# Kernel optimization log

Measured on AMD Instinct MI355X. Metric: run time of the kernel, lower is better.

## Reference

```python
import jax, jax.numpy as jnp
import numpy as np

N_FREQS = 6  # PositionEmbedding N_freqs when embedding=='pe'

def _pe(x):
    freqs = (2.0 ** jnp.arange(N_FREQS)).astype(x.dtype)
    fx = x * freqs  # [B,Q,N_FREQS]
    sc = jnp.stack([jnp.sin(fx), jnp.cos(fx)], axis=-1).reshape(fx.shape[0], fx.shape[1], 2 * N_FREQS)
    return jnp.concatenate([x, sc], axis=-1)

def _mlp(h, W1, b1, W2, b2, W3, b3):
    h = jax.nn.relu(h @ W1 + b1)
    h = jax.nn.relu(h @ W2 + b2)
    return h @ W3 + b3

def setup_inputs() -> dict:
    key = jax.random.key(0)
    B, Q, N, D, H = 4, 65536, 8192, 16, 128
    ks = jax.random.split(key, 6)
    coord = jax.random.uniform(ks[0], (B, Q, 1), minval=-1.0, maxval=1.0, dtype=jnp.float32)
    latent = jax.random.normal(ks[1], (B, N, D), dtype=jnp.float32)
    in_dim = (1 + 2 * N_FREQS) + 3 * D  # pe(rel_coord) ++ unfolded feat = 13 + 48 = 61
    def init(k, shp, fan):
        return (jax.random.normal(k, shp, dtype=jnp.float32) / np.float32(np.sqrt(fan)))
    W1 = init(ks[2], (in_dim, H), in_dim); b1 = jnp.zeros((H,), jnp.float32)
    W2 = init(ks[3], (H, H), H);          b2 = jnp.zeros((H,), jnp.float32)
    W3 = init(ks[4], (H, 1), H);          b3 = jnp.zeros((1,), jnp.float32)
    return dict(coord=coord, latent=latent, W1=W1, b1=b1, W2=W2, b2=b2, W3=W3, b3=b3)

def reference(coord, latent, W1, b1, W2, b2, W3, b3):
    B, Q, _ = coord.shape
    N = latent.shape[1]
    # feat_unfold: concat shifted-prev / self / shifted-next along feature dim -> [B,N,3D]
    prev = jnp.concatenate([latent[:, :1], latent[:, :-1]], axis=1)
    nxt = jnp.concatenate([latent[:, 1:], latent[:, -1:]], axis=1)
    feat = jnp.concatenate([prev, latent, nxt], axis=-1)
    # make_coord grid: cell centers in [-1,1]
    grid = (-1.0 + (2.0 * jnp.arange(N, dtype=coord.dtype) + 1.0) / N)
    rx = 1.0 / N           # 2/num_latents/2
    eps_shift = 1e-6
    preds, areas = [], []
    for vx in (-2.0, 0.0):  # eval path vx_lst
        c = jnp.clip(coord + vx * rx + eps_shift, -1.0 + 1e-6, 1.0 - 1e-6)
        idx = jnp.clip(jnp.searchsorted(grid, c[..., 0]), 0, N - 1)  # [B,Q]
        q_coord = grid[idx][..., None]                               # [B,Q,1]
        q_feat = jnp.take_along_axis(feat, idx[..., None], axis=1)   # [B,Q,3D]
        rel = (coord - q_coord) * N                                  # scaled rel coord
        area = jnp.abs(rel[..., 0]) + 1e-9                           # [B,Q]
        inp = jnp.concatenate([_pe(rel), q_feat], axis=-1)           # [B,Q,61]
        preds.append(_mlp(inp, W1, b1, W2, b2, W3, b3))              # [B,Q,1]
        areas.append(area)
    tot = areas[0] + areas[1]
    # local_ensemble: swap areas before weighting
    ret = preds[0] * (areas[1] / tot)[..., None] + preds[1] * (areas[0] / tot)[..., None]
    return ret
```

## Files before the change

kernel.cpp:

```cpp
#include <hip/hip_runtime.h>
#include <hip/hip_bf16.h>

typedef short s8v __attribute__((ext_vector_type(8)));
typedef float f4v __attribute__((ext_vector_type(4)));
typedef unsigned u4v __attribute__((ext_vector_type(4)));

__device__ __forceinline__ unsigned short f2bf(float x) {
  unsigned u = __builtin_bit_cast(unsigned, x);
  u += 0x7fffu + ((u >> 16) & 1u);
  return (unsigned short)(u >> 16);
}
__device__ __forceinline__ unsigned pk2(float a, float b) {
  unsigned ua = __builtin_bit_cast(unsigned, a) + 0x8000u;
  unsigned ub = __builtin_bit_cast(unsigned, b) + 0x8000u;
  return __builtin_amdgcn_perm(ub, ua, 0x07060302u);
}

__global__ void prep_kernel(const float* __restrict__ W1, const float* __restrict__ b1,
                            const float* __restrict__ W2, unsigned short* __restrict__ wsW) {
  int e = blockIdx.x * 256 + threadIdx.x;
  if (e < 8192) {
    int frag = e >> 9, rem = e & 511, lane = rem >> 3, j = rem & 7;
    int h = frag >> 1, ks = frag & 1;
    int q4 = lane >> 4, l15 = lane & 15;
    int k = ks * 32 + q4 * 8 + j;
    int n = h * 16 + l15;
    float v;
    if (k < 13) v = W1[k * 128 + n];
    else if (k == 13) v = b1[n];
    else if (k < 16) v = 0.0f;
    else v = W1[(k - 3) * 128 + n];
    wsW[e] = f2bf(v);
  } else {
    int e2 = e - 8192;
    int frag = e2 >> 9, rem = e2 & 511, lane = rem >> 3, j = rem & 7;
    int h2 = frag >> 2, ks = frag & 3;
    int q4 = lane >> 4, l15 = lane & 15;
    int kd = (j < 4) ? (32 * ks + 4 * q4 + j) : (32 * ks + 16 + 4 * q4 + (j - 4));
    int n = h2 * 16 + l15;
    wsW[e] = f2bf(W2[kd * 128 + n]);
  }
}

__global__ __launch_bounds__(256, 2) void lisagon_main(
    const float* __restrict__ coord, const float* __restrict__ latent,
    const unsigned short* __restrict__ W1f, const unsigned short* __restrict__ W2f,
    const float* __restrict__ b2, const float* __restrict__ W3,
    const float* __restrict__ b3, float* __restrict__ out) {
  __shared__ __align__(16) unsigned short A1[256 * 64];
  __shared__ float AREA[256];

  const int t = threadIdx.x;
  const int lane = t & 63, wv = t >> 6;
  const int l15 = lane & 15, q4 = lane >> 4;

  {
    const int r = t;
    const int Rg = blockIdx.x * 256 + r;
    const int gq = Rg >> 1, p = Rg & 1;
    const float co = coord[gq];
    float c = (co + (p ? 0.0f : -0.000244140625f)) + 1e-6f;
    c = fminf(fmaxf(c, -1.0f + 1e-6f), 1.0f - 1e-6f);
    double u = ((double)c * 8192.0 + 8191.0) * 0.5;
    int idx = (int)ceil(u);
    idx = min(max(idx, 0), 8191);

    float qc = ((float)(2 * idx + 1) - 8192.0f) * (1.0f / 8192.0f);
    float rel = (co - qc) * 8192.0f;
    AREA[r] = fabsf(rel) + 1e-9f;

    uint4* A1v = (uint4*)A1;
    const float4* latv = (const float4*)(latent + (size_t)(gq >> 16) * (8192 * 16));
    int rows3[3];
    rows3[0] = max(idx - 1, 0);
    rows3[1] = idx;
    rows3[2] = min(idx + 1, 8191);
    float4 L[3][4];
#pragma unroll
    for (int s = 0; s < 3; s++)
#pragma unroll
      for (int w = 0; w < 4; w++) L[s][w] = latv[rows3[s] * 4 + w];

    float v[16];
    v[0] = rel;
    float f = rel;
#pragma unroll
    for (int i = 0; i < 6; i++) {
      v[1 + 2 * i] = __sinf(f);
      v[2 + 2 * i] = __cosf(f);
      f = f + f;
    }
    v[13] = 1.0f;
    v[14] = 0.0f; v[15] = 0.0f;
#pragma unroll
    for (int ch = 0; ch < 2; ch++) {
      union { uint4 u4; unsigned us[4]; } pkv;
#pragma unroll
      for (int w = 0; w < 4; w++) pkv.us[w] = pk2(v[ch * 8 + 2 * w], v[ch * 8 + 2 * w + 1]);
      A1v[r * 8 + (ch ^ (r & 7))] = pkv.u4;
    }
#pragma unroll
    for (int s = 0; s < 3; s++) {
      union { uint4 u4; unsigned us[4]; } p0, p1;
      p0.us[0] = pk2(L[s][0].x, L[s][0].y); p0.us[1] = pk2(L[s][0].z, L[s][0].w);
      p0.us[2] = pk2(L[s][1].x, L[s][1].y); p0.us[3] = pk2(L[s][1].z, L[s][1].w);
      p1.us[0] = pk2(L[s][2].x, L[s][2].y); p1.us[1] = pk2(L[s][2].z, L[s][2].w);
      p1.us[2] = pk2(L[s][3].x, L[s][3].y); p1.us[3] = pk2(L[s][3].z, L[s][3].w);
      int ch0 = 2 + 2 * s;
      A1v[r * 8 + (ch0 ^ (r & 7))]       = p0.u4;
      A1v[r * 8 + ((ch0 + 1) ^ (r & 7))] = p1.u4;
    }
  }
  __syncthreads();

  const s8v* W1fv = (const s8v*)W1f;
  const s8v* W2fv = (const s8v*)W2f;
  const s8v* A1s  = (const s8v*)A1;
  const int rbase = wv * 64;

  s8v Bf[2][4];
#pragma unroll
  for (int ks = 0; ks < 2; ks++)
#pragma unroll
    for (int rt = 0; rt < 4; rt++) {
      int row = rbase + rt * 16 + l15;
      Bf[ks][rt] = A1s[row * 8 + ((ks * 4 + q4) ^ (row & 7))];
    }

  u4v bbv[4][4];
#pragma unroll
  for (int h = 0; h < 8; h++) {
    f4v a[4];
#pragma unroll
    for (int rt = 0; rt < 4; rt++) a[rt] = (f4v){0.f, 0.f, 0.f, 0.f};
#pragma unroll
    for (int ks = 0; ks < 2; ks++) {
      s8v Af = W1fv[(h * 2 + ks) * 64 + lane];
#pragma unroll
      for (int rt = 0; rt < 4; rt++)
        a[rt] = __builtin_amdgcn_mfma_f32_16x16x32_bf16(Af, Bf[ks][rt], a[rt], 0, 0, 0);
    }
#pragma unroll
    for (int rt = 0; rt < 4; rt++) {
      bbv[rt][h >> 1][2 * (h & 1)]     = pk2(fmaxf(a[rt][0], 0.f), fmaxf(a[rt][1], 0.f));
      bbv[rt][h >> 1][2 * (h & 1) + 1] = pk2(fmaxf(a[rt][2], 0.f), fmaxf(a[rt][3], 0.f));
    }
  }

  float s[4] = {0.f, 0.f, 0.f, 0.f};
#pragma unroll
  for (int h2 = 0; h2 < 8; h2++) {
    f4v a2[4];
    f4v b2v = ((const f4v*)b2)[h2 * 4 + q4];
#pragma unroll
    for (int rt = 0; rt < 4; rt++) a2[rt] = b2v;
#pragma unroll
    for (int ks = 0; ks < 4; ks++) {
      s8v Af = W2fv[(h2 * 4 + ks) * 64 + lane];
#pragma unroll
      for (int rt = 0; rt < 4; rt++)
        a2[rt] = __builtin_amdgcn_mfma_f32_16x16x32_bf16(
            Af, __builtin_bit_cast(s8v, bbv[rt][ks]), a2[rt], 0, 0, 0);
    }
    float4 w3v = ((const float4*)W3)[h2 * 4 + q4];
#pragma unroll
    for (int rt = 0; rt < 4; rt++) {
      s[rt] += fmaxf(a2[rt][0], 0.f) * w3v.x;
      s[rt] += fmaxf(a2[rt][1], 0.f) * w3v.y;
      s[rt] += fmaxf(a2[rt][2], 0.f) * w3v.z;
      s[rt] += fmaxf(a2[rt][3], 0.f) * w3v.w;
    }
  }

  const float b3s = b3[0];
#pragma unroll
  for (int rt = 0; rt < 4; rt++) {
    float pred = s[rt];
    pred += __shfl_xor(pred, 16, 64);
    pred += __shfl_xor(pred, 32, 64);
    pred += b3s;
    float other = __shfl_xor(pred, 1, 64);
    if (q4 == 0 && (l15 & 1) == 0) {
      int row0 = rbase + rt * 16 + l15;
      float a0 = AREA[row0], a1 = AREA[row0 + 1];
      float tot = a0 + a1;
      out[(blockIdx.x * 256 + row0) >> 1] = pred * (a1 / tot) + other * (a0 / tot);
    }
  }
}

extern "C" void kernel_launch(void* const* d_in, const int* in_sizes, int n_in,
                              void* d_out, int out_size, void* d_ws, size_t ws_size,
                              hipStream_t stream) {
  const float* coord  = (const float*)d_in[0];
  const float* latent = (const float*)d_in[1];
  const float* W1 = (const float*)d_in[2];
  const float* b1 = (const float*)d_in[3];
  const float* W2 = (const float*)d_in[4];
  const float* b2 = (const float*)d_in[5];
  const float* W3 = (const float*)d_in[6];
  const float* b3 = (const float*)d_in[7];
  float* out = (float*)d_out;
  unsigned short* wsW = (unsigned short*)d_ws;

  prep_kernel<<<96, 256, 0, stream>>>(W1, b1, W2, wsW);
  lisagon_main<<<2048, 256, 0, stream>>>(coord, latent, wsW, wsW + 8192,
                                         b2, W3, b3, out);
}
```

Baseline: 104.9 us.

## Switch MLP matmuls from 16x16x32 to 32x32x16 bf16 MFMA tiles

Replaces the 16x16x32 MFMA tiling of both hidden layers with 32x32x16 MFMA instructions. The weight-prep kernel and the register layouts for the layer-1 output, the bias, W3 and the final reduction are re-derived to match. Larger MFMA tiles mean fewer instructions and fewer weight-fragment loads per row, at the cost of more accumulator registers per wave and a less flexible layout that may affect occupancy.

```diff
diff --git a/kernel.cpp b/kernel.cpp
--- a/kernel.cpp
+++ b/kernel.cpp
@@ -2,7 +2,7 @@
 #include <hip/hip_bf16.h>
 
 typedef short s8v __attribute__((ext_vector_type(8)));
-typedef float f4v __attribute__((ext_vector_type(4)));
+typedef float f16v __attribute__((ext_vector_type(16)));
 typedef unsigned u4v __attribute__((ext_vector_type(4)));
 
 __device__ __forceinline__ unsigned short f2bf(float x) {
@@ -21,10 +21,10 @@
   int e = blockIdx.x * 256 + threadIdx.x;
   if (e < 8192) {
     int frag = e >> 9, rem = e & 511, lane = rem >> 3, j = rem & 7;
-    int h = frag >> 1, ks = frag & 1;
-    int q4 = lane >> 4, l15 = lane & 15;
-    int k = ks * 32 + q4 * 8 + j;
-    int n = h * 16 + l15;
+    int mt = frag >> 2, ks = frag & 3;
+    int half = lane >> 5, m = lane & 31;
+    int k = 16 * ks + 8 * half + j;
+    int n = 32 * mt + m;
     float v;
     if (k < 13) v = W1[k * 128 + n];
     else if (k == 13) v = b1[n];
@@ -34,11 +34,11 @@
   } else {
     int e2 = e - 8192;
     int frag = e2 >> 9, rem = e2 & 511, lane = rem >> 3, j = rem & 7;
-    int h2 = frag >> 2, ks = frag & 3;
-    int q4 = lane >> 4, l15 = lane & 15;
-    int kd = (j < 4) ? (32 * ks + 4 * q4 + j) : (32 * ks + 16 + 4 * q4 + (j - 4));
-    int n = h2 * 16 + l15;
-    wsW[e] = f2bf(W2[kd * 128 + n]);
+    int mt2 = frag >> 3, ks = frag & 7;
+    int half = lane >> 5, m = lane & 31;
+    int h = 32 * (ks >> 1) + 4 * half + (j & 3) + 8 * (j >> 2) + ((ks & 1) ? 16 : 0);
+    int n = 32 * mt2 + m;
+    wsW[e] = f2bf(W2[h * 128 + n]);
   }
 }
 
@@ -52,7 +52,7 @@
 
   const int t = threadIdx.x;
   const int lane = t & 63, wv = t >> 6;
-  const int l15 = lane & 15, q4 = lane >> 4;
+  const int l31 = lane & 31, half = lane >> 5;
 
   {
     const int r = t;
@@ -118,73 +118,86 @@
   const s8v* A1s  = (const s8v*)A1;
   const int rbase = wv * 64;
 
-  s8v Bf[2][4];
-#pragma unroll
-  for (int ks = 0; ks < 2; ks++)
-#pragma unroll
-    for (int rt = 0; rt < 4; rt++) {
-      int row = rbase + rt * 16 + l15;
-      Bf[ks][rt] = A1s[row * 8 + ((ks * 4 + q4) ^ (row & 7))];
-    }
-
-  u4v bbv[4][4];
-#pragma unroll
-  for (int h = 0; h < 8; h++) {
-    f4v a[4];
-#pragma unroll
-    for (int rt = 0; rt < 4; rt++) a[rt] = (f4v){0.f, 0.f, 0.f, 0.f};
-#pragma unroll
-    for (int ks = 0; ks < 2; ks++) {
-      s8v Af = W1fv[(h * 2 + ks) * 64 + lane];
-#pragma unroll
-      for (int rt = 0; rt < 4; rt++)
-        a[rt] = __builtin_amdgcn_mfma_f32_16x16x32_bf16(Af, Bf[ks][rt], a[rt], 0, 0, 0);
-    }
-#pragma unroll
-    for (int rt = 0; rt < 4; rt++) {
-      bbv[rt][h >> 1][2 * (h & 1)]     = pk2(fmaxf(a[rt][0], 0.f), fmaxf(a[rt][1], 0.f));
-      bbv[rt][h >> 1][2 * (h & 1) + 1] = pk2(fmaxf(a[rt][2], 0.f), fmaxf(a[rt][3], 0.f));
-    }
-  }
-
-  float s[4] = {0.f, 0.f, 0.f, 0.f};
-#pragma unroll
-  for (int h2 = 0; h2 < 8; h2++) {
-    f4v a2[4];
-    f4v b2v = ((const f4v*)b2)[h2 * 4 + q4];
-#pragma unroll
-    for (int rt = 0; rt < 4; rt++) a2[rt] = b2v;
+  s8v Bin[2][4];
+#pragma unroll
+  for (int nt = 0; nt < 2; nt++)
 #pragma unroll
     for (int ks = 0; ks < 4; ks++) {
-      s8v Af = W2fv[(h2 * 4 + ks) * 64 + lane];
-#pragma unroll
-      for (int rt = 0; rt < 4; rt++)
-        a2[rt] = __builtin_amdgcn_mfma_f32_16x16x32_bf16(
-            Af, __builtin_bit_cast(s8v, bbv[rt][ks]), a2[rt], 0, 0, 0);
-    }
-    float4 w3v = ((const float4*)W3)[h2 * 4 + q4];
-#pragma unroll
-    for (int rt = 0; rt < 4; rt++) {
-      s[rt] += fmaxf(a2[rt][0], 0.f) * w3v.x;
-      s[rt] += fmaxf(a2[rt][1], 0.f) * w3v.y;
-      s[rt] += fmaxf(a2[rt][2], 0.f) * w3v.z;
-      s[rt] += fmaxf(a2[rt][3], 0.f) * w3v.w;
+      int row = rbase + nt * 32 + l31;
+      int o = 2 * ks + half;
+      Bin[nt][ks] = A1s[row * 8 + (o ^ (row & 7))];
+    }
+
+  u4v bbv[2][8];
+#pragma unroll
+  for (int mt = 0; mt < 4; mt++) {
+    f16v a[2];
+#pragma unroll
+    for (int nt = 0; nt < 2; nt++) a[nt] = (f16v)0.0f;
+#pragma unroll
+    for (int ks = 0; ks < 4; ks++) {
+      s8v Af = W1fv[(mt * 4 + ks) * 64 + lane];
+#pragma unroll
+      for (int nt = 0; nt < 2; nt++)
+        a[nt] = __builtin_amdgcn_mfma_f32_32x32x16_bf16(Af, Bin[nt][ks], a[nt], 0, 0, 0);
+    }
+#pragma unroll
+    for (int nt = 0; nt < 2; nt++) {
+#pragma unroll
+      for (int w = 0; w < 4; w++) {
+        bbv[nt][2 * mt][w] =
+            pk2(fmaxf(a[nt][2 * w], 0.f), fmaxf(a[nt][2 * w + 1], 0.f));
+        bbv[nt][2 * mt + 1][w] =
+            pk2(fmaxf(a[nt][8 + 2 * w], 0.f), fmaxf(a[nt][9 + 2 * w], 0.f));
+      }
+    }
+  }
+
+  float s[2] = {0.f, 0.f};
+#pragma unroll
+  for (int mt2 = 0; mt2 < 4; mt2++) {
+    f16v a2i;
+#pragma unroll
+    for (int g = 0; g < 4; g++) {
+      float4 b2g = *(const float4*)(b2 + 32 * mt2 + 4 * half + 8 * g);
+      a2i[4 * g + 0] = b2g.x; a2i[4 * g + 1] = b2g.y;
+      a2i[4 * g + 2] = b2g.z; a2i[4 * g + 3] = b2g.w;
+    }
+    f16v a2[2];
+    a2[0] = a2i; a2[1] = a2i;
+#pragma unroll
+    for (int ks = 0; ks < 8; ks++) {
+      s8v Af = W2fv[(mt2 * 8 + ks) * 64 + lane];
+#pragma unroll
+      for (int nt = 0; nt < 2; nt++)
+        a2[nt] = __builtin_amdgcn_mfma_f32_32x32x16_bf16(
+            Af, __builtin_bit_cast(s8v, bbv[nt][ks]), a2[nt], 0, 0, 0);
+    }
+#pragma unroll
+    for (int g = 0; g < 4; g++) {
+      float4 w3g = *(const float4*)(W3 + 32 * mt2 + 4 * half + 8 * g);
+#pragma unroll
+      for (int nt = 0; nt < 2; nt++) {
+        s[nt] += fmaxf(a2[nt][4 * g + 0], 0.f) * w3g.x;
+        s[nt] += fmaxf(a2[nt][4 * g + 1], 0.f) * w3g.y;
+        s[nt] += fmaxf(a2[nt][4 * g + 2], 0.f) * w3g.z;
+        s[nt] += fmaxf(a2[nt][4 * g + 3], 0.f) * w3g.w;
+      }
     }
   }
 
   const float b3s = b3[0];
 #pragma unroll
-  for (int rt = 0; rt < 4; rt++) {
-    float pred = s[rt];
-    pred += __shfl_xor(pred, 16, 64);
+  for (int nt = 0; nt < 2; nt++) {
+    float pred = s[nt];
     pred += __shfl_xor(pred, 32, 64);
     pred += b3s;
     float other = __shfl_xor(pred, 1, 64);
-    if (q4 == 0 && (l15 & 1) == 0) {
-      int row0 = rbase + rt * 16 + l15;
-      float a0 = AREA[row0], a1 = AREA[row0 + 1];
+    if (half == 0 && (l31 & 1) == 0) {
+      int rloc = rbase + nt * 32 + l31;
+      float a0 = AREA[rloc], a1 = AREA[rloc + 1];
       float tot = a0 + a1;
-      out[(blockIdx.x * 256 + row0) >> 1] = pred * (a1 / tot) + other * (a0 / tot);
+      out[(blockIdx.x * 256 + rloc) >> 1] = pred * (a1 / tot) + other * (a0 / tot);
     }
   }
 }
```

Result: slower. 120.8 us (+15.1%).

## Pre-convert latent to bf16, stage W2 in LDS, use hardware bf16 pack

Applied to the files above, without the earlier changes.

The prep kernel now also converts the whole latent tensor to bf16 in the workspace, so the main kernel gathers half as many bytes per neighbour row and no longer packs them itself. W2 fragments are copied into shared memory with global_load_lds at kernel start, and the second-layer MFMA loop reads them from LDS instead of global memory. pk2 uses the hardware cvt_pk_bf16_f32 builtin when the compiler provides it. The cost is a larger prep launch that reads and writes all of latent, plus an extra 32 KB of LDS per block, which may limit blocks per CU. There is no explicit wait on the async LDS copy beyond the existing __syncthreads.

```diff
diff --git a/kernel.cpp b/kernel.cpp
--- a/kernel.cpp
+++ b/kernel.cpp
@@ -10,14 +10,27 @@
   u += 0x7fffu + ((u >> 16) & 1u);
   return (unsigned short)(u >> 16);
 }
+#if __has_builtin(__builtin_amdgcn_cvt_pk_bf16_f32)
+__device__ __forceinline__ unsigned pk2(float a, float b) {
+  return __builtin_bit_cast(unsigned, __builtin_amdgcn_cvt_pk_bf16_f32(a, b));
+}
+#else
 __device__ __forceinline__ unsigned pk2(float a, float b) {
   unsigned ua = __builtin_bit_cast(unsigned, a) + 0x8000u;
   unsigned ub = __builtin_bit_cast(unsigned, b) + 0x8000u;
   return __builtin_amdgcn_perm(ub, ua, 0x07060302u);
 }
+#endif
+
+__device__ __forceinline__ void g2lds16(const void* g, void* l) {
+  __builtin_amdgcn_global_load_lds(
+      (const __attribute__((address_space(1))) unsigned*)g,
+      (__attribute__((address_space(3))) unsigned*)l, 16, 0, 0);
+}
 
 __global__ void prep_kernel(const float* __restrict__ W1, const float* __restrict__ b1,
-                            const float* __restrict__ W2, unsigned short* __restrict__ wsW) {
+                            const float* __restrict__ W2, const float* __restrict__ latent,
+                            unsigned short* __restrict__ wsW) {
   int e = blockIdx.x * 256 + threadIdx.x;
   if (e < 8192) {
     int frag = e >> 9, rem = e & 511, lane = rem >> 3, j = rem & 7;
@@ -31,7 +44,7 @@
     else if (k < 16) v = 0.0f;
     else v = W1[(k - 3) * 128 + n];
     wsW[e] = f2bf(v);
-  } else {
+  } else if (e < 24576) {
     int e2 = e - 8192;
     int frag = e2 >> 9, rem = e2 & 511, lane = rem >> 3, j = rem & 7;
     int h2 = frag >> 2, ks = frag & 3;
@@ -39,20 +52,30 @@
     int kd = (j < 4) ? (32 * ks + 4 * q4 + j) : (32 * ks + 16 + 4 * q4 + (j - 4));
     int n = h2 * 16 + l15;
     wsW[e] = f2bf(W2[kd * 128 + n]);
+  } else {
+    int i = e - 24576;
+    wsW[e] = f2bf(latent[i]);
   }
 }
 
 __global__ __launch_bounds__(256, 2) void lisagon_main(
-    const float* __restrict__ coord, const float* __restrict__ latent,
+    const float* __restrict__ coord, const unsigned short* __restrict__ latbf,
     const unsigned short* __restrict__ W1f, const unsigned short* __restrict__ W2f,
     const float* __restrict__ b2, const float* __restrict__ W3,
     const float* __restrict__ b3, float* __restrict__ out) {
   __shared__ __align__(16) unsigned short A1[256 * 64];
+  __shared__ __align__(16) unsigned short W2s[16384];
   __shared__ float AREA[256];
 
   const int t = threadIdx.x;
   const int lane = t & 63, wv = t >> 6;
   const int l15 = lane & 15, q4 = lane >> 4;
+
+#pragma unroll
+  for (int it = 0; it < 8; it++) {
+    int off = (it * 4 + wv) * 1024;
+    g2lds16((const char*)W2f + off + lane * 16, (char*)W2s + off);
+  }
 
   {
     const int r = t;
@@ -70,16 +93,17 @@
     AREA[r] = fabsf(rel) + 1e-9f;
 
     uint4* A1v = (uint4*)A1;
-    const float4* latv = (const float4*)(latent + (size_t)(gq >> 16) * (8192 * 16));
+    const uint4* latv = (const uint4*)(latbf + (size_t)(gq >> 16) * (8192 * 16));
     int rows3[3];
     rows3[0] = max(idx - 1, 0);
     rows3[1] = idx;
     rows3[2] = min(idx + 1, 8191);
-    float4 L[3][4];
-#pragma unroll
-    for (int s = 0; s < 3; s++)
-#pragma unroll
-      for (int w = 0; w < 4; w++) L[s][w] = latv[rows3[s] * 4 + w];
+    uint4 L0[3], L1[3];
+#pragma unroll
+    for (int s = 0; s < 3; s++) {
+      L0[s] = latv[rows3[s] * 2 + 0];
+      L1[s] = latv[rows3[s] * 2 + 1];
+    }
 
     float v[16];
     v[0] = rel;
@@ -101,20 +125,15 @@
     }
 #pragma unroll
     for (int s = 0; s < 3; s++) {
-      union { uint4 u4; unsigned us[4]; } p0, p1;
-      p0.us[0] = pk2(L[s][0].x, L[s][0].y); p0.us[1] = pk2(L[s][0].z, L[s][0].w);
-      p0.us[2] = pk2(L[s][1].x, L[s][1].y); p0.us[3] = pk2(L[s][1].z, L[s][1].w);
-      p1.us[0] = pk2(L[s][2].x, L[s][2].y); p1.us[1] = pk2(L[s][2].z, L[s][2].w);
-      p1.us[2] = pk2(L[s][3].x, L[s][3].y); p1.us[3] = pk2(L[s][3].z, L[s][3].w);
       int ch0 = 2 + 2 * s;
-      A1v[r * 8 + (ch0 ^ (r & 7))]       = p0.u4;
-      A1v[r * 8 + ((ch0 + 1) ^ (r & 7))] = p1.u4;
+      A1v[r * 8 + (ch0 ^ (r & 7))]       = L0[s];
+      A1v[r * 8 + ((ch0 + 1) ^ (r & 7))] = L1[s];
     }
   }
   __syncthreads();
 
   const s8v* W1fv = (const s8v*)W1f;
-  const s8v* W2fv = (const s8v*)W2f;
+  const s8v* W2sv = (const s8v*)W2s;
   const s8v* A1s  = (const s8v*)A1;
   const int rbase = wv * 64;
 
@@ -156,7 +175,7 @@
     for (int rt = 0; rt < 4; rt++) a2[rt] = b2v;
 #pragma unroll
     for (int ks = 0; ks < 4; ks++) {
-      s8v Af = W2fv[(h2 * 4 + ks) * 64 + lane];
+      s8v Af = W2sv[(h2 * 4 + ks) * 64 + lane];
 #pragma unroll
       for (int rt = 0; rt < 4; rt++)
         a2[rt] = __builtin_amdgcn_mfma_f32_16x16x32_bf16(
@@ -203,7 +222,7 @@
   float* out = (float*)d_out;
   unsigned short* wsW = (unsigned short*)d_ws;
 
-  prep_kernel<<<96, 256, 0, stream>>>(W1, b1, W2, wsW);
-  lisagon_main<<<2048, 256, 0, stream>>>(coord, latent, wsW, wsW + 8192,
+  prep_kernel<<<2144, 256, 0, stream>>>(W1, b1, W2, latent, wsW);
+  lisagon_main<<<2048, 256, 0, stream>>>(coord, wsW + 24576, wsW, wsW + 8192,
                                          b2, W3, b3, out);
 }
```

Measured after the change: 100.4 us. 4.3% less time.
